# Performance work log

Measured on AMD Instinct MI355X. Metric: run time of the kernel, lower is better.

## Reference

```python
import jax, jax.numpy as jnp
import numpy as np

N_NODES = 100000
D = 128
N_EDGES = 800000


def setup_inputs() -> dict:
    key = jax.random.key(0)
    k_feat, k_src, k_dst, k_ws, k_wn = jax.random.split(key, 5)
    scale = 1.0 / np.sqrt(D)
    return {
        "features": jax.random.normal(k_feat, (N_NODES, D), jnp.float32),
        "src": jax.random.randint(k_src, (N_EDGES,), 0, N_NODES, jnp.int32),
        "dst": jax.random.randint(k_dst, (N_EDGES,), 0, N_NODES, jnp.int32),
        "gamma": jnp.ones((D,), jnp.float32),
        "beta": jnp.zeros((D,), jnp.float32),
        "W_self": jax.random.normal(k_ws, (D, D), jnp.float32) * scale,
        "W_neigh": jax.random.normal(k_wn, (D, D), jnp.float32) * scale,
        "b": jnp.zeros((D,), jnp.float32),
    }


def reference(features, src, dst, gamma, beta, W_self, W_neigh, b):
    n = features.shape[0]
    eps = 1e-5
    # BatchNorm1d (training mode: batch stats over the node dim, biased var)
    mean = jnp.mean(features, axis=0)
    var = jnp.mean(jnp.square(features - mean), axis=0)
    h = (features - mean) * jax.lax.rsqrt(var + eps) * gamma + beta  # [N, D]

    # SAGEConv 'mean': gather source feats along edges, mean-reduce per dst node
    msg = h[src]  # [E, D] irregular gather
    agg = jax.ops.segment_sum(msg, dst, num_segments=n)  # [N, D]
    deg = jax.ops.segment_sum(jnp.ones(src.shape, h.dtype), dst, num_segments=n)
    h_neigh = agg / jnp.maximum(deg, 1.0)[:, None]  # zero-degree nodes stay 0

    conv = h @ W_self + h_neigh @ W_neigh + b  # fc_self + fc_neigh + bias
    out = conv + h  # skip connection
    return jax.nn.gelu(out, approximate=False)
```

## Files before the change

kernel.cpp:

```cpp
#include <hip/hip_runtime.h>

#define DD 128
#define NPB_LOG 8
#define NPB 256
#define EPB 2048

typedef __attribute__((ext_vector_type(8))) short short8;
typedef __attribute__((ext_vector_type(4))) float f32x4;
typedef __attribute__((ext_vector_type(2))) float f32x2;

__device__ inline unsigned short f2bf(float f) {
    unsigned u = __float_as_uint(f);
    unsigned r = u + 0x7fffu + ((u >> 16) & 1u);
    return (unsigned short)(r >> 16);
}

__global__ __launch_bounds__(256) void phase1_k(
    const float4* __restrict__ x, float* __restrict__ stats16, int n,
    const int* __restrict__ dst, int nE, int NCHUNK, int NBUCK,
    const float* __restrict__ Wself, const float* __restrict__ Wneigh,
    unsigned short* __restrict__ Bpre, int* __restrict__ cm) {
    int b = blockIdx.x, tid = threadIdx.x;
    __shared__ float ls[8][256];
    if (b < NCHUNK) {
        int chunk = b;
        int* cnt = (int*)ls;
        for (int i = tid; i < NBUCK; i += 256) cnt[i] = 0;
        __syncthreads();
        int e0 = chunk * EPB;
#pragma unroll
        for (int j = 0; j < 8; ++j) {
            int e = e0 + j * 256 + tid;
            if (e < nE) atomicAdd(&cnt[dst[e] >> NPB_LOG], 1);
        }
        __syncthreads();
        for (int bk = tid; bk < NBUCK; bk += 256)
            cm[(size_t)bk * NCHUNK + chunk] = cnt[bk];
    } else if (b < NCHUNK + 16) {
        int q = (b - NCHUNK) * 256 + tid;
        int l = q & 63;
        int kb = ((q >> 9) << 5) + ((l >> 4) << 3);
        int nn = (((q >> 6) & 7) << 4) + (l & 15);
        bool self = (kb < 128);
        const float* Wp = self ? (Wself + (size_t)kb * 128 + nn)
                               : (Wneigh + (size_t)(kb - 128) * 128 + nn);
        unsigned tmp[4];
#pragma unroll
        for (int j = 0; j < 4; ++j) {
            float v0 = Wp[(2 * j) * 128];
            float v1 = Wp[(2 * j + 1) * 128];
            if (self) {
                if (kb + 2 * j == nn) v0 += 1.0f;
                if (kb + 2 * j + 1 == nn) v1 += 1.0f;
            }
            tmp[j] = (unsigned)f2bf(v0) | ((unsigned)f2bf(v1) << 16);
        }
        uint4 w; w.x = tmp[0]; w.y = tmp[1]; w.z = tmp[2]; w.w = tmp[3];
        *(uint4*)(Bpre + (size_t)q * 8) = w;
    } else {
        int bb = b - NCHUNK - 16;
        int c4 = tid & 31, sub = tid >> 5;
        float sx = 0.f, sy = 0.f, sz = 0.f, sw = 0.f;
        float qx = 0.f, qy = 0.f, qz = 0.f, qw = 0.f;
        for (int r = bb * 8 + sub; r < n; r += 1024 * 8) {
            float4 v = x[(size_t)r * 32 + c4];
            sx += v.x; sy += v.y; sz += v.z; sw += v.w;
            qx += v.x * v.x; qy += v.y * v.y; qz += v.z * v.z; qw += v.w * v.w;
        }
        ls[sub][c4 * 4 + 0] = sx; ls[sub][c4 * 4 + 1] = sy;
        ls[sub][c4 * 4 + 2] = sz; ls[sub][c4 * 4 + 3] = sw;
        ls[sub][128 + c4 * 4 + 0] = qx; ls[sub][128 + c4 * 4 + 1] = qy;
        ls[sub][128 + c4 * 4 + 2] = qz; ls[sub][128 + c4 * 4 + 3] = qw;
        __syncthreads();
        float t = 0.f;
#pragma unroll
        for (int k = 0; k < 8; ++k) t += ls[k][tid];
        atomicAdd(&stats16[(bb & 15) * 256 + tid], t);
    }
}

__global__ __launch_bounds__(256) void scanF_k(
    const int* __restrict__ v_in, unsigned long long* __restrict__ desc,
    int* __restrict__ out, int nCM,
    const float* __restrict__ stats16, const float* __restrict__ gamma,
    const float* __restrict__ beta, float* __restrict__ scsh, float inv_n) {
    int b = blockIdx.x, t = threadIdx.x;
    if (b == 0 && t < 128) {
        float s = 0.f, q = 0.f;
#pragma unroll
        for (int sh = 0; sh < 16; ++sh) {
            s += stats16[sh * 256 + t];
            q += stats16[sh * 256 + 128 + t];
        }
        float mean = s * inv_n;
        float var = q * inv_n - mean * mean;
        float sc = rsqrtf(var + 1e-5f) * gamma[t];
        scsh[t] = sc;
        scsh[128 + t] = beta[t] - mean * sc;
    }
    int i0 = b * 1024 + t * 4;
    int4 v = {0, 0, 0, 0};
    if (i0 + 3 < nCM) v = *(const int4*)(v_in + i0);
    else {
        if (i0 < nCM) v.x = v_in[i0];
        if (i0 + 1 < nCM) v.y = v_in[i0 + 1];
        if (i0 + 2 < nCM) v.z = v_in[i0 + 2];
    }
    int s4 = v.x + v.y + v.z + v.w;
    __shared__ int ls[256];
    __shared__ int sExcl;
    ls[t] = s4;
    __syncthreads();
#pragma unroll
    for (int off = 1; off < 256; off <<= 1) {
        int x = (t >= off) ? ls[t - off] : 0;
        __syncthreads();
        ls[t] += x;
        __syncthreads();
    }
    if (t == 0) {
        int blockTotal = ls[255];
        __hip_atomic_store(&desc[b], (1ull << 32) | (unsigned)blockTotal,
                           __ATOMIC_RELEASE, __HIP_MEMORY_SCOPE_AGENT);
        int excl = 0;
        for (int i = b - 1; i >= 0;) {
            unsigned long long d;
            do {
                d = __hip_atomic_load(&desc[i], __ATOMIC_ACQUIRE,
                                      __HIP_MEMORY_SCOPE_AGENT);
            } while ((d >> 32) == 0ull);
            excl += (int)(unsigned)d;
            if ((d >> 32) == 2ull) break;
            --i;
        }
        __hip_atomic_store(&desc[b],
                           (2ull << 32) | (unsigned)(excl + blockTotal),
                           __ATOMIC_RELEASE, __HIP_MEMORY_SCOPE_AGENT);
        sExcl = excl;
    }
    __syncthreads();
    int run = sExcl + ((t == 0) ? 0 : ls[t - 1]);
    int4 o;
    o.x = run; o.y = run + v.x; o.z = o.y + v.y; o.w = o.z + v.z;
    if (i0 + 3 < nCM) *(int4*)(out + i0) = o;
    else {
        if (i0 < nCM) out[i0] = o.x;
        if (i0 + 1 < nCM) out[i0 + 1] = o.y;
        if (i0 + 2 < nCM) out[i0 + 2] = o.z;
    }
}

__global__ __launch_bounds__(256) void phase2_k(
    const float4* __restrict__ x, const float* __restrict__ scsh,
    uint2* __restrict__ hbuf, unsigned* __restrict__ h8, int n,
    const int* __restrict__ src, const int* __restrict__ dst,
    const int* __restrict__ cmscan, unsigned* __restrict__ pairs,
    int nE, int NCHUNK, int NBUCK) {
    int b = blockIdx.x, tid = threadIdx.x;
    __shared__ int a[512];
    __shared__ int lcur[512];
    __shared__ int bas[512];
    __shared__ unsigned lsorted[EPB];
    __shared__ unsigned short lbk[EPB];
    if (b < NCHUNK) {
        int chunk = b;
        int e0 = chunk * EPB;
        int nv = min(EPB, nE - e0);
        for (int i = tid; i < 512; i += 256) a[i] = 0;
        __syncthreads();
        int myd[8];
#pragma unroll
        for (int j = 0; j < 8; ++j) {
            int e = e0 + j * 256 + tid;
            int d = (e < nE) ? dst[e] : -1;
            myd[j] = d;
            if (d >= 0) atomicAdd(&a[d >> NPB_LOG], 1);
        }
        for (int bk = tid; bk < NBUCK; bk += 256)
            bas[bk] = cmscan[(size_t)bk * NCHUNK + chunk];
        __syncthreads();
        for (int d = 1; d < 512; d <<= 1) {
            int idx = (tid + 1) * (d << 1) - 1;
            if (idx < 512) a[idx] += a[idx - d];
            __syncthreads();
        }
        if (tid == 0) a[511] = 0;
        __syncthreads();
        for (int d = 256; d >= 1; d >>= 1) {
            int idx = (tid + 1) * (d << 1) - 1;
            if (idx < 512) { int tm = a[idx - d]; a[idx - d] = a[idx]; a[idx] += tm; }
            __syncthreads();
        }
        for (int i = tid; i < 512; i += 256) lcur[i] = a[i];
        __syncthreads();
#pragma unroll
        for (int j = 0; j < 8; ++j) {
            int d = myd[j];
            if (d >= 0) {
                int e = e0 + j * 256 + tid;
                int bk = d >> NPB_LOG;
                int lp = atomicAdd(&lcur[bk], 1);
                lsorted[lp] = ((unsigned)src[e] << NPB_LOG) | (unsigned)(d & (NPB - 1));
                lbk[lp] = (unsigned short)bk;
            }
        }
        __syncthreads();
        for (int i = tid; i < nv; i += 256) {
            int bk = lbk[i];
            pairs[bas[bk] + i - a[bk]] = lsorted[i];
        }
    } else {
        int blk = b - NCHUNK;
        int c4 = tid & 31, sub = tid >> 5;
        int r0 = blk * 16 + sub, r1 = r0 + 8;
        float4 sc = ((const float4*)scsh)[c4];
        float4 sh = ((const float4*)(scsh + 128))[c4];
        bool ok0 = r0 < n, ok1 = r1 < n;
        float4 v0, v1;
        if (ok0) v0 = x[(size_t)r0 * 32 + c4];
        if (ok1) v1 = x[(size_t)r1 * 32 + c4];
        if (ok0) {
            float hx = v0.x * sc.x + sh.x, hy = v0.y * sc.y + sh.y;
            float hz = v0.z * sc.z + sh.z, hw = v0.w * sc.w + sh.w;
            uint2 o;
            o.x = (unsigned)f2bf(hx) | ((unsigned)f2bf(hy) << 16);
            o.y = (unsigned)f2bf(hz) | ((unsigned)f2bf(hw) << 16);
            hbuf[(size_t)r0 * 32 + c4] = o;
            int p8 = __builtin_amdgcn_cvt_pk_fp8_f32(hx, hy, 0, false);
            p8 = __builtin_amdgcn_cvt_pk_fp8_f32(hz, hw, p8, true);
            h8[(size_t)r0 * 32 + c4] = (unsigned)p8;
        }
        if (ok1) {
            float hx = v1.x * sc.x + sh.x, hy = v1.y * sc.y + sh.y;
            float hz = v1.z * sc.z + sh.z, hw = v1.w * sc.w + sh.w;
            uint2 o;
            o.x = (unsigned)f2bf(hx) | ((unsigned)f2bf(hy) << 16);
            o.y = (unsigned)f2bf(hz) | ((unsigned)f2bf(hw) << 16);
            hbuf[(size_t)r1 * 32 + c4] = o;
            int p8 = __builtin_amdgcn_cvt_pk_fp8_f32(hx, hy, 0, false);
            p8 = __builtin_amdgcn_cvt_pk_fp8_f32(hz, hw, p8, true);
            h8[(size_t)r1 * 32 + c4] = (unsigned)p8;
        }
    }
}

__global__ __launch_bounds__(256) void sortC_k(
    const unsigned* __restrict__ pairs, const int* __restrict__ cmscan,
    int* __restrict__ offsets, int* __restrict__ csr,
    int n, int nE, int NCHUNK, int NBUCK) {
    int b = blockIdx.x, tid = threadIdx.x;
    int base0 = cmscan[(size_t)b * NCHUNK];
    int end = (b + 1 < NBUCK) ? cmscan[(size_t)(b + 1) * NCHUNK] : nE;
    __shared__ int cnt[NPB];
    __shared__ int cur[NPB];
    cnt[tid] = 0;
    __syncthreads();
    for (int e = base0 + tid; e < end; e += 256)
        atomicAdd(&cnt[pairs[e] & (NPB - 1)], 1);
    __syncthreads();
    int c0 = cnt[tid];
    __shared__ int ps[256];
    ps[tid] = c0;
    __syncthreads();
#pragma unroll
    for (int off = 1; off < 256; off <<= 1) {
        int v = (tid >= off) ? ps[tid - off] : 0;
        __syncthreads();
        ps[tid] += v;
        __syncthreads();
    }
    int ex = base0 + ps[tid] - c0;
    cur[tid] = ex;
    int node = b * NPB + tid;
    if (node < n) offsets[node] = ex;
    if (b == NBUCK - 1 && tid == 0) offsets[n] = nE;
    __syncthreads();
    for (int e = base0 + tid; e < end; e += 256) {
        unsigned u = pairs[e];
        int p = atomicAdd(&cur[u & (NPB - 1)], 1);
        csr[p] = (int)(u >> NPB_LOG);
    }
}

#define ACC8(v)                                                       \
    do {                                                              \
        acc[0] += __builtin_amdgcn_cvt_pk_f32_fp8((v).x, false);      \
        acc[1] += __builtin_amdgcn_cvt_pk_f32_fp8((v).x, true);       \
        acc[2] += __builtin_amdgcn_cvt_pk_f32_fp8((v).y, false);      \
        acc[3] += __builtin_amdgcn_cvt_pk_f32_fp8((v).y, true);       \
        acc[4] += __builtin_amdgcn_cvt_pk_f32_fp8((v).z, false);      \
        acc[5] += __builtin_amdgcn_cvt_pk_f32_fp8((v).z, true);       \
        acc[6] += __builtin_amdgcn_cvt_pk_f32_fp8((v).w, false);      \
        acc[7] += __builtin_amdgcn_cvt_pk_f32_fp8((v).w, true);       \
    } while (0)

__global__ __launch_bounds__(256) void pull_k(
    const int* __restrict__ offsets, const int* __restrict__ csr,
    const uint4* __restrict__ h8q, uint4* __restrict__ hnw, int n) {
    int wv = (blockIdx.x * 256 + threadIdx.x) >> 6;
    int lane = threadIdx.x & 63;
    int g = lane >> 3, sl = lane & 7;
    int node = wv * 8 + g;
    bool valid = node < n;
    int nc = valid ? node : (n - 1);
    int b0 = offsets[nc], b1 = offsets[nc + 1];
    f32x2 acc[8];
#pragma unroll
    for (int k = 0; k < 8; ++k) acc[k] = f32x2{0.f, 0.f};
    int j = b0;
    for (; j + 4 <= b1; j += 4) {
        int i0 = csr[j], i1 = csr[j + 1], i2 = csr[j + 2], i3 = csr[j + 3];
        uint4 v0 = h8q[(size_t)i0 * 8 + sl];
        uint4 v1 = h8q[(size_t)i1 * 8 + sl];
        uint4 v2 = h8q[(size_t)i2 * 8 + sl];
        uint4 v3 = h8q[(size_t)i3 * 8 + sl];
        ACC8(v0); ACC8(v1); ACC8(v2); ACC8(v3);
    }
    if (j + 2 <= b1) {
        int i0 = csr[j], i1 = csr[j + 1];
        uint4 v0 = h8q[(size_t)i0 * 8 + sl];
        uint4 v1 = h8q[(size_t)i1 * 8 + sl];
        ACC8(v0); ACC8(v1);
        j += 2;
    }
    if (j < b1) {
        int i0 = csr[j];
        uint4 v0 = h8q[(size_t)i0 * 8 + sl];
        ACC8(v0);
    }
    if (valid) {
        float rd = (b1 > b0) ? 1.0f / (float)(b1 - b0) : 0.0f;
        unsigned ow[8];
#pragma unroll
        for (int k = 0; k < 8; ++k)
            ow[k] = (unsigned)f2bf(acc[k].x * rd) |
                    ((unsigned)f2bf(acc[k].y * rd) << 16);
        uint4 o1; o1.x = ow[0]; o1.y = ow[1]; o1.z = ow[2]; o1.w = ow[3];
        uint4 o2; o2.x = ow[4]; o2.y = ow[5]; o2.z = ow[6]; o2.w = ow[7];
        hnw[(size_t)node * 16 + sl * 2] = o1;
        hnw[(size_t)node * 16 + sl * 2 + 1] = o2;
    }
}

__global__ __launch_bounds__(256, 2) void gemm_k(
    const unsigned short* __restrict__ h, const unsigned short* __restrict__ hn,
    const unsigned short* __restrict__ Bpre, const float* __restrict__ bias,
    float* __restrict__ out, int n) {
    __shared__ unsigned short Bsw[32768];
    int tid = threadIdx.x, wave = tid >> 6, lane = tid & 63;
    int rb = blockIdx.x;
#pragma unroll
    for (int i = 0; i < 16; ++i) {
        int g = wave * 16 + i;
        __builtin_amdgcn_global_load_lds(
            (const __attribute__((address_space(1))) void*)(
                Bpre + ((size_t)g * 64 + lane) * 8),
            (__attribute__((address_space(3))) void*)(Bsw + (size_t)g * 512),
            16, 0, 0);
    }
    __syncthreads();

    int quad = lane >> 4, mrow = lane & 15;
    int r0 = rb * 128 + wave * 32;
    int rA0 = min(r0 + mrow, n - 1);
    int rA1 = min(r0 + 16 + mrow, n - 1);

    f32x4 zero = {0.0f, 0.0f, 0.0f, 0.0f};
    f32x4 acc[2][8];
#pragma unroll
    for (int m = 0; m < 2; ++m)
#pragma unroll
        for (int t = 0; t < 8; ++t) acc[m][t] = zero;

#pragma unroll
    for (int s = 0; s < 8; ++s) {
        int kb = s * 32 + quad * 8;
        short8 a0, a1;
        if (s < 4) {
            a0 = *(const short8*)(h + (size_t)rA0 * 128 + kb);
            a1 = *(const short8*)(h + (size_t)rA1 * 128 + kb);
        } else {
            int kk = kb - 128;
            a0 = *(const short8*)(hn + (size_t)rA0 * 128 + kk);
            a1 = *(const short8*)(hn + (size_t)rA1 * 128 + kk);
        }
#pragma unroll
        for (int tt = 0; tt < 8; ++tt) {
            short8 b = *(const short8*)(Bsw + ((size_t)(s * 8 + tt) * 64 + lane) * 8);
            acc[0][tt] = __builtin_amdgcn_mfma_f32_16x16x32_bf16(a0, b, acc[0][tt], 0, 0, 0);
            acc[1][tt] = __builtin_amdgcn_mfma_f32_16x16x32_bf16(a1, b, acc[1][tt], 0, 0, 0);
        }
    }

    float bi[8];
#pragma unroll
    for (int t = 0; t < 8; ++t) bi[t] = bias[t * 16 + mrow];
#pragma unroll
    for (int m = 0; m < 2; ++m) {
#pragma unroll
        for (int i = 0; i < 4; ++i) {
            int row = r0 + m * 16 + quad * 4 + i;
            if (row < n) {
#pragma unroll
                for (int t = 0; t < 8; ++t) {
                    int col = t * 16 + mrow;
                    float xv = acc[m][t][i] + bi[t];
                    float x2 = xv * xv;
                    float u = 0.7978845608f * xv * (1.0f + 0.044715f * x2);
                    float e = __expf(2.0f * u);
                    float th = 1.0f - 2.0f * __builtin_amdgcn_rcpf(e + 1.0f);
                    out[(size_t)row * 128 + col] = 0.5f * xv * (1.0f + th);
                }
            }
        }
    }
}

extern "C" void kernel_launch(void* const* d_in, const int* in_sizes, int n_in,
                              void* d_out, int out_size, void* d_ws, size_t ws_size,
                              hipStream_t stream) {
    const float* features = (const float*)d_in[0];
    const int* src = (const int*)d_in[1];
    const int* dst = (const int*)d_in[2];
    const float* gamma = (const float*)d_in[3];
    const float* beta = (const float*)d_in[4];
    const float* Wself = (const float*)d_in[5];
    const float* Wneigh = (const float*)d_in[6];
    const float* bias = (const float*)d_in[7];
    int n = in_sizes[0] / DD;
    int nE = in_sizes[1];
    int NCHUNK = (nE + EPB - 1) / EPB;
    int NBUCK = (n + NPB - 1) / NPB;
    int CM = NBUCK * NCHUNK;
    int tilesCM = (CM + 1023) / 1024;
    int nbNorm16 = (n + 15) / 16;

    auto align1k = [](size_t x) { return (x + 1023) & ~(size_t)1023; };
    char* ws = (char*)d_ws;
    size_t off = 0;
    float* stats16 = (float*)(ws + off);       off += 16384;
    unsigned long long* desc = (unsigned long long*)(ws + off); off += 2048;
    size_t zeroBytes = off;
    float* scsh   = (float*)(ws + off);        off += 2048;
    int* cm       = (int*)(ws + off);          off += align1k((size_t)CM * 4);
    int* cmscan   = (int*)(ws + off);          off += align1k((size_t)CM * 4);
    int* offsets  = (int*)(ws + off);          off += align1k((size_t)(n + 1) * 4);
    int* csr      = (int*)(ws + off);          off += align1k((size_t)nE * 4);
    unsigned* pairs = (unsigned*)(ws + off);   off += align1k((size_t)nE * 4);
    unsigned short* Bpre = (unsigned short*)(ws + off); off += 65536;
    unsigned short* hbuf = (unsigned short*)(ws + off); off += (size_t)n * 256;
    unsigned short* hnbuf = (unsigned short*)(ws + off); off += (size_t)n * 256;
    unsigned* h8 = (unsigned*)(ws + off);      off += (size_t)n * 128;

    hipMemsetAsync(stats16, 0, zeroBytes, stream);

    phase1_k<<<NCHUNK + 16 + 1024, 256, 0, stream>>>(
        (const float4*)features, stats16, n, dst, nE, NCHUNK, NBUCK,
        Wself, Wneigh, Bpre, cm);
    scanF_k<<<tilesCM, 256, 0, stream>>>(cm, desc, cmscan, CM,
                                         stats16, gamma, beta, scsh,
                                         1.0f / (float)n);
    phase2_k<<<NCHUNK + nbNorm16, 256, 0, stream>>>(
        (const float4*)features, scsh, (uint2*)hbuf, h8, n,
        src, dst, cmscan, pairs, nE, NCHUNK, NBUCK);
    sortC_k<<<NBUCK, 256, 0, stream>>>(pairs, cmscan, offsets, csr, n, nE,
                                       NCHUNK, NBUCK);
    {
        int waves = (n + 7) / 8;
        int blocks = (waves * 64 + 255) / 256;
        pull_k<<<blocks, 256, 0, stream>>>(
            offsets, csr, (const uint4*)h8, (uint4*)hnbuf, n);
    }
    gemm_k<<<(n + 127) / 128, 256, 0, stream>>>(
        hbuf, hnbuf, Bpre, bias, (float*)d_out, n);
}
```

Baseline: 214.7 us.

## Replace decoupled-lookback scan with per-bucket row scans using bucket totals

```diff
diff --git a/kernel.cpp b/kernel.cpp
--- a/kernel.cpp
+++ b/kernel.cpp
@@ -19,7 +19,8 @@
     const float4* __restrict__ x, float* __restrict__ stats16, int n,
     const int* __restrict__ dst, int nE, int NCHUNK, int NBUCK,
     const float* __restrict__ Wself, const float* __restrict__ Wneigh,
-    unsigned short* __restrict__ Bpre, int* __restrict__ cm) {
+    unsigned short* __restrict__ Bpre, int* __restrict__ cm,
+    int* __restrict__ bt) {
     int b = blockIdx.x, tid = threadIdx.x;
     __shared__ float ls[8][256];
     if (b < NCHUNK) {
@@ -34,8 +35,11 @@
             if (e < nE) atomicAdd(&cnt[dst[e] >> NPB_LOG], 1);
         }
         __syncthreads();
-        for (int bk = tid; bk < NBUCK; bk += 256)
-            cm[(size_t)bk * NCHUNK + chunk] = cnt[bk];
+        for (int bk = tid; bk < NBUCK; bk += 256) {
+            int c = cnt[bk];
+            cm[(size_t)bk * NCHUNK + chunk] = c;
+            if (c) atomicAdd(&bt[bk], c);
+        }
     } else if (b < NCHUNK + 16) {
         int q = (b - NCHUNK) * 256 + tid;
         int l = q & 63;
@@ -79,9 +83,9 @@
     }
 }
 
-__global__ __launch_bounds__(256) void scanF_k(
-    const int* __restrict__ v_in, unsigned long long* __restrict__ desc,
-    int* __restrict__ out, int nCM,
+__global__ __launch_bounds__(256) void scanR_k(
+    const int* __restrict__ cm, const int* __restrict__ bt,
+    int* __restrict__ cmscan, int NCHUNK, int NBUCK,
     const float* __restrict__ stats16, const float* __restrict__ gamma,
     const float* __restrict__ beta, float* __restrict__ scsh, float inv_n) {
     int b = blockIdx.x, t = threadIdx.x;
@@ -98,56 +102,40 @@
         scsh[t] = sc;
         scsh[128 + t] = beta[t] - mean * sc;
     }
-    int i0 = b * 1024 + t * 4;
-    int4 v = {0, 0, 0, 0};
-    if (i0 + 3 < nCM) v = *(const int4*)(v_in + i0);
-    else {
-        if (i0 < nCM) v.x = v_in[i0];
-        if (i0 + 1 < nCM) v.y = v_in[i0 + 1];
-        if (i0 + 2 < nCM) v.z = v_in[i0 + 2];
-    }
-    int s4 = v.x + v.y + v.z + v.w;
-    __shared__ int ls[256];
-    __shared__ int sExcl;
-    ls[t] = s4;
-    __syncthreads();
-#pragma unroll
-    for (int off = 1; off < 256; off <<= 1) {
-        int x = (t >= off) ? ls[t - off] : 0;
-        __syncthreads();
-        ls[t] += x;
-        __syncthreads();
-    }
-    if (t == 0) {
-        int blockTotal = ls[255];
-        __hip_atomic_store(&desc[b], (1ull << 32) | (unsigned)blockTotal,
-                           __ATOMIC_RELEASE, __HIP_MEMORY_SCOPE_AGENT);
-        int excl = 0;
-        for (int i = b - 1; i >= 0;) {
-            unsigned long long d;
-            do {
-                d = __hip_atomic_load(&desc[i], __ATOMIC_ACQUIRE,
-                                      __HIP_MEMORY_SCOPE_AGENT);
-            } while ((d >> 32) == 0ull);
-            excl += (int)(unsigned)d;
-            if ((d >> 32) == 2ull) break;
-            --i;
-        }
-        __hip_atomic_store(&desc[b],
-                           (2ull << 32) | (unsigned)(excl + blockTotal),
-                           __ATOMIC_RELEASE, __HIP_MEMORY_SCOPE_AGENT);
-        sExcl = excl;
-    }
-    __syncthreads();
-    int run = sExcl + ((t == 0) ? 0 : ls[t - 1]);
-    int4 o;
-    o.x = run; o.y = run + v.x; o.z = o.y + v.y; o.w = o.z + v.z;
-    if (i0 + 3 < nCM) *(int4*)(out + i0) = o;
-    else {
-        if (i0 < nCM) out[i0] = o.x;
-        if (i0 + 1 < nCM) out[i0 + 1] = o.y;
-        if (i0 + 2 < nCM) out[i0 + 2] = o.z;
-    }
+    __shared__ int a[512];
+    for (int i = t; i < 512; i += 256) a[i] = (i < NBUCK) ? bt[i] : 0;
+    __syncthreads();
+    for (int d = 1; d < 512; d <<= 1) {
+        int idx = (t + 1) * (d << 1) - 1;
+        if (idx < 512) a[idx] += a[idx - d];
+        __syncthreads();
+    }
+    if (t == 0) a[511] = 0;
+    __syncthreads();
+    for (int d = 256; d >= 1; d >>= 1) {
+        int idx = (t + 1) * (d << 1) - 1;
+        if (idx < 512) { int tm = a[idx - d]; a[idx - d] = a[idx]; a[idx] += tm; }
+        __syncthreads();
+    }
+    int base = a[b];
+    __syncthreads();
+    for (int i = t; i < 512; i += 256)
+        a[i] = (i < NCHUNK) ? cm[(size_t)b * NCHUNK + i] : 0;
+    __syncthreads();
+    for (int d = 1; d < 512; d <<= 1) {
+        int idx = (t + 1) * (d << 1) - 1;
+        if (idx < 512) a[idx] += a[idx - d];
+        __syncthreads();
+    }
+    if (t == 0) a[511] = 0;
+    __syncthreads();
+    for (int d = 256; d >= 1; d >>= 1) {
+        int idx = (t + 1) * (d << 1) - 1;
+        if (idx < 512) { int tm = a[idx - d]; a[idx - d] = a[idx]; a[idx] += tm; }
+        __syncthreads();
+    }
+    for (int c = t; c < NCHUNK; c += 256)
+        cmscan[(size_t)b * NCHUNK + c] = base + a[c];
 }
 
 __global__ __launch_bounds__(256) void phase2_k(
@@ -432,14 +420,13 @@
     int NCHUNK = (nE + EPB - 1) / EPB;
     int NBUCK = (n + NPB - 1) / NPB;
     int CM = NBUCK * NCHUNK;
-    int tilesCM = (CM + 1023) / 1024;
     int nbNorm16 = (n + 15) / 16;
 
     auto align1k = [](size_t x) { return (x + 1023) & ~(size_t)1023; };
     char* ws = (char*)d_ws;
     size_t off = 0;
     float* stats16 = (float*)(ws + off);       off += 16384;
-    unsigned long long* desc = (unsigned long long*)(ws + off); off += 2048;
+    int* bt       = (int*)(ws + off);          off += 2048;
     size_t zeroBytes = off;
     float* scsh   = (float*)(ws + off);        off += 2048;
     int* cm       = (int*)(ws + off);          off += align1k((size_t)CM * 4);
@@ -456,10 +443,10 @@
 
     phase1_k<<<NCHUNK + 16 + 1024, 256, 0, stream>>>(
         (const float4*)features, stats16, n, dst, nE, NCHUNK, NBUCK,
-        Wself, Wneigh, Bpre, cm);
-    scanF_k<<<tilesCM, 256, 0, stream>>>(cm, desc, cmscan, CM,
-                                         stats16, gamma, beta, scsh,
-                                         1.0f / (float)n);
+        Wself, Wneigh, Bpre, cm, bt);
+    scanR_k<<<NBUCK, 256, 0, stream>>>(cm, bt, cmscan, NCHUNK, NBUCK,
+                                       stats16, gamma, beta, scsh,
+                                       1.0f / (float)n);
     phase2_k<<<NCHUNK + nbNorm16, 256, 0, stream>>>(
         (const float4*)features, scsh, (uint2*)hbuf, h8, n,
         src, dst, cmscan, pairs, nE, NCHUNK, NBUCK);
```

New measurement: 197.2 us. -8.2%, faster.
